# Performance work log

Hardware: AMD Instinct MI355X
Metric: run time of the kernel (lower is better)

## Reference

```python
import jax, jax.numpy as jnp
import numpy as np

N = 50000      # nodes
IN = 128       # in_dim
HID = 128      # hidden_dim
HEADS = 4
OUT = HID // HEADS   # per-head out_channels
R = 8          # num_relations
E = 640000     # message-passing edges
E2 = 200000    # decode edge pairs
NC = 8         # num_classes
EPS_LN = 1e-5


def layer_norm(x, g, b):
    m = x.mean(-1, keepdims=True)
    v = ((x - m) ** 2).mean(-1, keepdims=True)
    return (x - m) * jax.lax.rsqrt(v + EPS_LN) * g + b


def rgat_conv(x, edge_index, edge_type, W, q, k, b):
    # PyG RGATConv defaults: additive-self-attention, across-relation softmax,
    # concat=True, negative_slope=0.2, sum aggregation.
    src, dst = edge_index[0], edge_index[1]
    # relation-specific transform for all nodes, then gather per edge
    xw = jnp.einsum('ni,rio->nro', x, W)          # [N, R, HID]
    xi = xw[dst, edge_type]                        # [E, HID] target feats
    xj = xw[src, edge_type]                        # [E, HID] source feats
    alpha = jax.nn.leaky_relu(xi @ q + xj @ k, negative_slope=0.2)  # [E, HEADS]
    # softmax over incoming edges of each destination node (per head)
    amax = jax.ops.segment_max(alpha, dst, num_segments=N)
    amax = jnp.where(jnp.isfinite(amax), amax, 0.0)
    ex = jnp.exp(alpha - amax[dst])
    den = jax.ops.segment_sum(ex, dst, num_segments=N)
    attn = ex / (den[dst] + 1e-16)                 # [E, HEADS]
    msg = (xj.reshape(E, HEADS, OUT) * attn[:, :, None]).reshape(E, HID)
    out = jax.ops.segment_sum(msg, dst, num_segments=N)  # [N, HID]
    return out + b


def setup_inputs() -> dict:
    key = jax.random.key(0)
    ks = jax.random.split(key, 12)
    sI = 1.0 / np.sqrt(IN)
    sH = 1.0 / np.sqrt(HID)
    return {
        'x': jax.random.normal(ks[0], (N, IN), jnp.float32),
        'edge_index': jax.random.randint(ks[1], (2, E), 0, N),
        'edge_type': jax.random.randint(ks[2], (E,), 0, R),
        'edges': jax.random.randint(ks[3], (E2, 2), 0, N),
        'w1': jax.random.normal(ks[4], (R, IN, HID), jnp.float32) * sI,
        'q1': jax.random.normal(ks[5], (HID, HEADS), jnp.float32) * sH,
        'k1': jax.random.normal(ks[6], (HID, HEADS), jnp.float32) * sH,
        'b1': jnp.zeros((HID,), jnp.float32),
        'w2': jax.random.normal(ks[7], (R, HID, HID), jnp.float32) * sH,
        'q2': jax.random.normal(ks[8], (HID, HEADS), jnp.float32) * sH,
        'k2': jax.random.normal(ks[9], (HID, HEADS), jnp.float32) * sH,
        'b2': jnp.zeros((HID,), jnp.float32),
        'ln1_g': jnp.ones((HID,), jnp.float32),
        'ln1_b': jnp.zeros((HID,), jnp.float32),
        'ln2_g': jnp.ones((HID,), jnp.float32),
        'ln2_b': jnp.zeros((HID,), jnp.float32),
        'mw1': jax.random.normal(ks[10], (2 * HID, HID), jnp.float32) / np.sqrt(2 * HID),
        'mb1': jnp.zeros((HID,), jnp.float32),
        'mw2': jax.random.normal(ks[11], (HID, NC), jnp.float32) * sH,
        'mb2': jnp.zeros((NC,), jnp.float32),
    }


def reference(x, edge_index, edge_type, edges,
              w1, q1, k1, b1, w2, q2, k2, b2,
              ln1_g, ln1_b, ln2_g, ln2_b,
              mw1, mb1, mw2, mb2):
    # encode (dropout is identity in eval mode)
    h1 = rgat_conv(x, edge_index, edge_type, w1, q1, k1, b1)
    h1 = layer_norm(jax.nn.relu(h1), ln1_g, ln1_b)
    h2 = rgat_conv(h1, edge_index, edge_type, w2, q2, k2, b2)
    h2 = layer_norm(jax.nn.relu(h2), ln2_g, ln2_b)
    h = h1 + h2
    # decode: gather node pairs, concat, MLP
    z = jnp.concatenate([h[edges[:, 0]], h[edges[:, 1]]], axis=1)  # [E2, 2*HID]
    z = jax.nn.gelu(z @ mw1 + mb1, approximate=False)
    return z @ mw2 + mb2  # [E2, NC]
```

## Files before the change

### kernel.cpp

```cpp
#include <hip/hip_runtime.h>
#include <hip/hip_bf16.h>

#define NN    50000
#define RR    8
#define HIDC  128
#define NHEADS 4
#define EE    640000
#define EE2   200000
#define NCL   8

typedef __hip_bfloat16 bf16;
typedef unsigned short u16;
typedef __attribute__((ext_vector_type(8))) short short8;
typedef __attribute__((ext_vector_type(4))) float floatx4;

__device__ __forceinline__ float us2f(u16 u) {
    return __uint_as_float(((unsigned)u) << 16);
}
__device__ __forceinline__ float bf2f(bf16 v) { return __bfloat162float(v); }
__device__ __forceinline__ u16 f2us(float f) {
    bf16 h = __float2bfloat16(f);
    return *(u16*)&h;
}
__device__ __forceinline__ float ldf(const void* p, int i, bool f32) {
    return f32 ? ((const float*)p)[i] : us2f(((const u16*)p)[i]);
}
__device__ __forceinline__ float wredmax(float v) {
#pragma unroll
    for (int off = 32; off; off >>= 1) v = fmaxf(v, __shfl_xor(v, off));
    return v;
}
__device__ __forceinline__ float wredsum(float v) {
#pragma unroll
    for (int off = 32; off; off >>= 1) v += __shfl_xor(v, off);
    return v;
}

__global__ __launch_bounds__(1024) void k_sniff(const u16* __restrict__ x, int* __restrict__ flags) {
    __shared__ int cnt;
    if (threadIdx.x == 0) cnt = 0;
    __syncthreads();
    int c = 0;
#pragma unroll
    for (int it = 0; it < 8; it++) {
        ushort4 a = ((const ushort4*)x)[(it * 1024 + threadIdx.x) * 2];
        ushort4 b = ((const ushort4*)x)[(it * 1024 + threadIdx.x) * 2 + 1];
        c += (((a.x >> 7) & 0xFF) == 0xFF) + (((a.y >> 7) & 0xFF) == 0xFF)
           + (((a.z >> 7) & 0xFF) == 0xFF) + (((a.w >> 7) & 0xFF) == 0xFF)
           + (((b.x >> 7) & 0xFF) == 0xFF) + (((b.y >> 7) & 0xFF) == 0xFF)
           + (((b.z >> 7) & 0xFF) == 0xFF) + (((b.w >> 7) & 0xFF) == 0xFF);
    }
    c += __shfl_xor(c, 32); c += __shfl_xor(c, 16); c += __shfl_xor(c, 8);
    c += __shfl_xor(c, 4);  c += __shfl_xor(c, 2);  c += __shfl_xor(c, 1);
    if ((threadIdx.x & 63) == 0) atomicAdd(&cnt, c);
    __syncthreads();
    if (threadIdx.x == 0) { flags[0] = (cnt > 16) ? 1 : 0; flags[1] = 0; }
}

__global__ void k_zero(int* __restrict__ p, int n) {
    int i = blockIdx.x * 256 + threadIdx.x;
    if (i < n) p[i] = 0;
}
__global__ void k_hist(const int* __restrict__ ei, int* __restrict__ deg) {
    int e = blockIdx.x * 256 + threadIdx.x;
    if (e < EE) atomicAdd(&deg[ei[EE + e]], 1);
}
__global__ __launch_bounds__(256) void k_scan1(const int* __restrict__ deg,
                                               int* __restrict__ bsum) {
    int i = blockIdx.x * 256 + threadIdx.x;
    int v = (i < NN) ? deg[i] : 0;
    __shared__ int red[4];
    int lane = threadIdx.x & 63, w = threadIdx.x >> 6;
#pragma unroll
    for (int off = 32; off; off >>= 1) v += __shfl_xor(v, off);
    if (lane == 0) red[w] = v;
    __syncthreads();
    if (threadIdx.x == 0) bsum[blockIdx.x] = red[0] + red[1] + red[2] + red[3];
}
__global__ __launch_bounds__(256) void k_scan2(const int* __restrict__ bsum,
                                               int* __restrict__ boff,
                                               int* __restrict__ rowptr) {
    __shared__ int s[256];
    int t = threadIdx.x;
    s[t] = (t < 196) ? bsum[t] : 0;
    __syncthreads();
    for (int off = 1; off < 256; off <<= 1) {
        int u = (t >= off) ? s[t - off] : 0;
        __syncthreads();
        s[t] += u;
        __syncthreads();
    }
    if (t < 196) boff[t] = (t == 0) ? 0 : s[t - 1];
    if (t == 255) rowptr[NN] = s[255];
}
__global__ __launch_bounds__(256) void k_scan3(int* __restrict__ deg ,
                                               const int* __restrict__ boff,
                                               int* __restrict__ rowptr) {
    __shared__ int s[256];
    int t = threadIdx.x;
    int i = blockIdx.x * 256 + t;
    int v = (i < NN) ? deg[i] : 0;
    s[t] = v;
    __syncthreads();
    for (int off = 1; off < 256; off <<= 1) {
        int u = (t >= off) ? s[t - off] : 0;
        __syncthreads();
        s[t] += u;
        __syncthreads();
    }
    if (i < NN) {
        int val = boff[blockIdx.x] + s[t] - v;
        rowptr[i] = val;
        deg[i] = val;
    }
}
__global__ void k_scatter(const int* __restrict__ ei, int* __restrict__ cursor,
                          int* __restrict__ elist) {
    int e = blockIdx.x * 256 + threadIdx.x;
    if (e >= EE) return;
    int pos = atomicAdd(&cursor[ei[EE + e]], 1);
    elist[pos] = e;
}

__global__ void k_qkw(const void* __restrict__ w1, const void* __restrict__ w2,
                      const void* __restrict__ q1, const void* __restrict__ k1,
                      const void* __restrict__ q2, const void* __restrict__ k2,
                      float* __restrict__ qkw, const int* __restrict__ fl) {
    int idx = blockIdx.x * 256 + threadIdx.x;
    if (idx >= 16384) return;
    const bool f = fl[0] != 0;
    int mat = idx >> 10;
    int i   = (idx >> 3) & 127;
    int h8  = idx & 7;
    const void* W = (mat >= 8) ? w2 : w1;
    const void* qk = (mat >= 8) ? ((h8 < 4) ? q2 : k2) : ((h8 < 4) ? q1 : k1);
    int h = h8 & 3;
    int r = mat & 7;
    float acc = 0.f;
    for (int o = 0; o < HIDC; o++)
        acc += ldf(W, (r * HIDC + i) * HIDC + o, f) * ldf(qk, o * NHEADS + h, f);
    qkw[idx] = acc;
}

__global__ void k_wswz(const void* __restrict__ w1, const void* __restrict__ w2,
                       const float* __restrict__ qkw,
                       u16* __restrict__ Wf2, const int* __restrict__ fl) {
    int idx = blockIdx.x * 256 + threadIdx.x;
    if (idx >= 36864) return;
    const bool f = fl[0] != 0;
    int mat = idx / 2304, rest = idx % 2304;
    int c = rest >> 8, q = (rest >> 6) & 3, ln = rest & 63;
    int k0 = q * 32 + (ln >> 4) * 8;
    int nn = c * 16 + (ln & 15);
    int r = mat & 7;
    u16 o[8];
    if (c < 8) {
        const void* W = (mat >= 8) ? w2 : w1;
#pragma unroll
        for (int j = 0; j < 8; j++)
            o[j] = f2us(ldf(W, (r * HIDC + k0 + j) * HIDC + nn, f));
    } else {
        int col = nn - 128;
#pragma unroll
        for (int j = 0; j < 8; j++)
            o[j] = (col < 8) ? f2us(qkw[mat * 1024 + (k0 + j) * 8 + col]) : (u16)0;
    }
    u16* dst = Wf2 + (size_t)mat * 18432 + (size_t)(((c * 4 + q) * 64 + ln) * 8);
    *(ushort4*)dst       = ushort4{o[0], o[1], o[2], o[3]};
    *(ushort4*)(dst + 4) = ushort4{o[4], o[5], o[6], o[7]};
}

__global__ __launch_bounds__(512) void k_xw2(const void* __restrict__ X,
                                             const u16* __restrict__ Wf2,
                                             bf16* __restrict__ xw,
                                             float* __restrict__ sbuf,
                                             float* __restrict__ tbuf,
                                             const int* __restrict__ fx,
                                             int layer) {
    __shared__ u16 Xs[64 * 136];
    __shared__ u16 Os[8][16 * 136];
    const int tid = threadIdx.x;
    const int n0 = blockIdx.x * 64;
    const bool xf = fx[0] != 0;
    for (int v = tid; v < 2048; v += 512) {
        int row = v >> 5, c4 = (v & 31) * 4, n = n0 + row;
        ushort4 o = {0, 0, 0, 0};
        if (n < NN) {
            if (xf) {
                float4 hv = *(const float4*)((const float*)X + (size_t)n * HIDC + c4);
                o = ushort4{f2us(hv.x), f2us(hv.y), f2us(hv.z), f2us(hv.w)};
            } else {
                o = *(const ushort4*)((const u16*)X + (size_t)n * HIDC + c4);
            }
        }
        *(ushort4*)&Xs[row * 136 + c4] = o;
    }
    __syncthreads();
    const int w = tid >> 6, lane = tid & 63;
    const int wr = w & 3;
    const int rh = w >> 2;
    short8 af[4];
#pragma unroll
    for (int q = 0; q < 4; q++)
        af[q] = *(const short8*)&Xs[(16 * wr + (lane & 15)) * 136 + q * 32 + (lane >> 4) * 8];
    u16* Ow = Os[w];
    for (int rr = 0; rr < 4; rr++) {
        const int r = rh * 4 + rr;
        const u16* Wfr = Wf2 + (size_t)(layer * 8 + r) * 18432;
#pragma unroll
        for (int c = 0; c < 9; c++) {
            floatx4 acc = {0.f, 0.f, 0.f, 0.f};
#pragma unroll
            for (int q = 0; q < 4; q++) {
                short8 bfr = *(const short8*)&Wfr[(size_t)(((c * 4 + q) * 64 + lane) * 8)];
                acc = __builtin_amdgcn_mfma_f32_16x16x32_bf16(af[q], bfr, acc, 0, 0, 0);
            }
            if (c < 8) {
                int col = c * 16 + (lane & 15);
#pragma unroll
                for (int reg = 0; reg < 4; reg++) {
                    int lp = (lane >> 4) * 4 + reg;
                    Ow[lp * 136 + col] = f2us(acc[reg]);
                }
            } else {
                int cl = lane & 15;
                if (cl < 8) {
                    float* dstp = (cl < 4) ? sbuf : tbuf;
                    int h = cl & 3;
#pragma unroll
                    for (int reg = 0; reg < 4; reg++) {
                        int p = 16 * wr + (lane >> 4) * 4 + reg;
                        int n = n0 + p;
                        if (n < NN) dstp[(size_t)(n * RR + r) * 4 + h] = acc[reg];
                    }
                }
            }
        }
#pragma unroll
        for (int i = 0; i < 4; i++) {
            int v = i * 64 + lane;
            int lrow = v >> 4;
            int c8 = (v & 15) * 8;
            int n = n0 + 16 * wr + lrow;
            if (n < NN) {
                short8 hv = *(const short8*)&Ow[lrow * 136 + c8];
                *(short8*)((u16*)xw + (size_t)(n * RR + r) * HIDC + c8) = hv;
            }
        }
    }
}

__global__ __launch_bounds__(256) void k_attn(const int* __restrict__ rowptr,
                                              const int* __restrict__ elist,
                                              const int* __restrict__ ei,
                                              const int* __restrict__ et,
                                              const float* __restrict__ sb,
                                              const float* __restrict__ tb,
                                              const bf16* __restrict__ xw,
                                              const void* __restrict__ b,
                                              const void* __restrict__ g,
                                              const void* __restrict__ bb,
                                              const u16* __restrict__ hprev,
                                              u16* __restrict__ hout,
                                              const int* __restrict__ fl) {
    const int lane = threadIdx.x & 63;
    const int d = blockIdx.x * 4 + (threadIdx.x >> 6);
    if (d >= NN) return;
    const bool f = fl[0] != 0;
    const int half = lane >> 5;
    const int sl = lane & 31;
    const int hh = sl >> 3;
    const int start = rowptr[d], end = rowptr[d + 1];
    float m0 = -1e30f, m1 = -1e30f, m2 = -1e30f, m3 = -1e30f;
    float l0 = 0.f, l1 = 0.f, l2 = 0.f, l3 = 0.f;
    float acc0 = 0.f, acc1 = 0.f, acc2 = 0.f, acc3 = 0.f;
    for (int c0 = start; c0 < end; c0 += 64) {
        int n = end - c0;
        if (n > 64) n = 64;
        float a0, a1, a2, a3;
        int sr = 0;
        if (lane < n) {
            int e = elist[c0 + lane];
            int src = ei[e], r = et[e];
            sr = src * RR + r;
            float4 si = *(const float4*)&sb[(size_t)(d * RR + r) * 4];
            float4 tj = *(const float4*)&tb[(size_t)sr * 4];
            a0 = si.x + tj.x; a0 = a0 >= 0.f ? a0 : 0.2f * a0;
            a1 = si.y + tj.y; a1 = a1 >= 0.f ? a1 : 0.2f * a1;
            a2 = si.z + tj.z; a2 = a2 >= 0.f ? a2 : 0.2f * a2;
            a3 = si.w + tj.w; a3 = a3 >= 0.f ? a3 : 0.2f * a3;
        } else { a0 = a1 = a2 = a3 = -1e30f; }
        float n0 = fmaxf(m0, wredmax(a0));
        float n1 = fmaxf(m1, wredmax(a1));
        float n2 = fmaxf(m2, wredmax(a2));
        float n3 = fmaxf(m3, wredmax(a3));
        float s0 = __expf(m0 - n0), s1 = __expf(m1 - n1);
        float s2 = __expf(m2 - n2), s3 = __expf(m3 - n3);
        float e0 = __expf(a0 - n0), e1 = __expf(a1 - n1);
        float e2 = __expf(a2 - n2), e3 = __expf(a3 - n3);
        l0 = l0 * s0 + wredsum(e0);
        l1 = l1 * s1 + wredsum(e1);
        l2 = l2 * s2 + wredsum(e2);
        l3 = l3 * s3 + wredsum(e3);
        float scl = hh == 0 ? s0 : hh == 1 ? s1 : hh == 2 ? s2 : s3;
        acc0 *= scl; acc1 *= scl; acc2 *= scl; acc3 *= scl;
        for (int j2 = 0; j2 < n; j2 += 2) {
            int jl = j2 + half;
            int srj = __shfl(sr, jl);
            float wx = __shfl(e0, jl), wy = __shfl(e1, jl);
            float wz = __shfl(e2, jl), ww = __shfl(e3, jl);
            float wgt = hh == 0 ? wx : hh == 1 ? wy : hh == 2 ? wz : ww;
            ushort4 u = *(const ushort4*)((const u16*)xw + (size_t)srj * HIDC + sl * 4);
            acc0 += wgt * us2f(u.x);
            acc1 += wgt * us2f(u.y);
            acc2 += wgt * us2f(u.z);
            acc3 += wgt * us2f(u.w);
        }
        m0 = n0; m1 = n1; m2 = n2; m3 = n3;
    }
    acc0 += __shfl_xor(acc0, 32);
    acc1 += __shfl_xor(acc1, 32);
    acc2 += __shfl_xor(acc2, 32);
    acc3 += __shfl_xor(acc3, 32);
    float ld = hh == 0 ? l0 : hh == 1 ? l1 : hh == 2 ? l2 : l3;
    float inv = 1.f / (ld + 1e-16f);
    float v0 = fmaxf(acc0 * inv + ldf(b, sl * 4 + 0, f), 0.f);
    float v1 = fmaxf(acc1 * inv + ldf(b, sl * 4 + 1, f), 0.f);
    float v2 = fmaxf(acc2 * inv + ldf(b, sl * 4 + 2, f), 0.f);
    float v3 = fmaxf(acc3 * inv + ldf(b, sl * 4 + 3, f), 0.f);
    float sum = v0 + v1 + v2 + v3;
#pragma unroll
    for (int off = 16; off; off >>= 1) sum += __shfl_xor(sum, off);
    float mean = sum * (1.f / 128.f);
    v0 -= mean; v1 -= mean; v2 -= mean; v3 -= mean;
    float sq = v0 * v0 + v1 * v1 + v2 * v2 + v3 * v3;
#pragma unroll
    for (int off = 16; off; off >>= 1) sq += __shfl_xor(sq, off);
    float rstd = rsqrtf(sq * (1.f / 128.f) + 1e-5f);
    if (half == 0) {
        float y0 = v0 * rstd * ldf(g, sl * 4 + 0, f) + ldf(bb, sl * 4 + 0, f);
        float y1 = v1 * rstd * ldf(g, sl * 4 + 1, f) + ldf(bb, sl * 4 + 1, f);
        float y2 = v2 * rstd * ldf(g, sl * 4 + 2, f) + ldf(bb, sl * 4 + 2, f);
        float y3 = v3 * rstd * ldf(g, sl * 4 + 3, f) + ldf(bb, sl * 4 + 3, f);
        if (hprev) {
            ushort4 hv = *(const ushort4*)&hprev[(size_t)d * HIDC + sl * 4];
            y0 += us2f(hv.x); y1 += us2f(hv.y); y2 += us2f(hv.z); y3 += us2f(hv.w);
        }
        ushort4 o = {f2us(y0), f2us(y1), f2us(y2), f2us(y3)};
        *(ushort4*)&hout[(size_t)d * HIDC + sl * 4] = o;
    }
}

__global__ void k_dswz(const void* __restrict__ mw1, const void* __restrict__ mw2,
                       u16* __restrict__ Wf, const int* __restrict__ fl) {
    int idx = blockIdx.x * 256 + threadIdx.x;
    if (idx >= 4352) return;
    const bool f = fl[0] != 0;
    u16 o[8];
    if (idx < 4096) {
        int c = idx >> 9, q = (idx >> 6) & 7, ln = idx & 63;
        int k0 = q * 32 + (ln >> 4) * 8;
        int nn = c * 16 + (ln & 15);
#pragma unroll
        for (int j = 0; j < 8; j++)
            o[j] = f2us(ldf(mw1, (k0 + j) * HIDC + nn, f));
    } else {
        int fidx = idx - 4096;
        int q = fidx >> 6, ln = fidx & 63;
        int k0 = q * 32 + (ln >> 4) * 8;
        int nn = ln & 15;
#pragma unroll
        for (int j = 0; j < 8; j++)
            o[j] = (nn < 8) ? f2us(ldf(mw2, (k0 + j) * NCL + nn, f)) : (u16)0;
    }
    *(ushort4*)&Wf[idx * 8]     = ushort4{o[0], o[1], o[2], o[3]};
    *(ushort4*)&Wf[idx * 8 + 4] = ushort4{o[4], o[5], o[6], o[7]};
}

__global__ __launch_bounds__(256) void k_decode2(const u16* __restrict__ h,
                                                 const int* __restrict__ edges,
                                                 const u16* __restrict__ Wf,
                                                 const void* __restrict__ mb1,
                                                 const void* __restrict__ mb2,
                                                 void* __restrict__ out,
                                                 const int* __restrict__ fl) {
    __shared__ u16 zsu[64 * 136];
    const int tid = threadIdx.x;
    const bool f = fl[0] != 0;
    const int p0 = blockIdx.x * 64;
    const int w = tid >> 6, lane = tid & 63;
    const int m = 16 * w + (lane & 15);
    const int g = lane >> 4;
    const int na = edges[(size_t)(p0 + m) * 2];
    const int nb = edges[(size_t)(p0 + m) * 2 + 1];
    short8 af[8];
#pragma unroll
    for (int q = 0; q < 8; q++) {
        int k0 = q * 32 + g * 8;
        af[q] = *(const short8*)(h + (size_t)((k0 >> 7) ? nb : na) * HIDC + (k0 & 127));
    }
#pragma unroll
    for (int c = 0; c < 8; c++) {
        floatx4 acc = {0.f, 0.f, 0.f, 0.f};
#pragma unroll
        for (int q = 0; q < 8; q++) {
            short8 bfr = *(const short8*)&Wf[(size_t)(((c * 8 + q) * 64 + lane) * 8)];
            acc = __builtin_amdgcn_mfma_f32_16x16x32_bf16(af[q], bfr, acc, 0, 0, 0);
        }
        int col = c * 16 + (lane & 15);
        float bv = ldf(mb1, col, f);
#pragma unroll
        for (int reg = 0; reg < 4; reg++) {
            int p = 16 * w + (lane >> 4) * 4 + reg;
            float z = acc[reg] + bv;
            zsu[p * 136 + col] = f2us(0.5f * z * (1.f + erff(z * 0.70710678118654752f)));
        }
    }
    floatx4 acc2 = {0.f, 0.f, 0.f, 0.f};
#pragma unroll
    for (int q = 0; q < 4; q++) {
        short8 af2 = *(const short8*)&zsu[m * 136 + q * 32 + g * 8];
        short8 bfr2 = *(const short8*)&Wf[32768 + (size_t)((q * 64 + lane) * 8)];
        acc2 = __builtin_amdgcn_mfma_f32_16x16x32_bf16(af2, bfr2, acc2, 0, 0, 0);
    }
    int col16 = lane & 15;
    if (col16 < 8) {
        float bv2 = ldf(mb2, col16, f);
#pragma unroll
        for (int reg = 0; reg < 4; reg++) {
            int p = 16 * w + (lane >> 4) * 4 + reg;
            float sv = acc2[reg] + bv2;
            size_t oi = (size_t)(p0 + p) * NCL + col16;
            if (f) ((float*)out)[oi] = sv;
            else   ((bf16*)out)[oi] = __float2bfloat16(sv);
        }
    }
}

extern "C" void kernel_launch(void* const* d_in, const int* in_sizes, int n_in,
                              void* d_out, int out_size, void* d_ws, size_t ws_size,
                              hipStream_t stream) {
    (void)in_sizes; (void)n_in; (void)out_size; (void)ws_size;
    const void* x    = d_in[0];
    const int* ei    = (const int*)d_in[1];
    const int* et    = (const int*)d_in[2];
    const int* edges = (const int*)d_in[3];
    const void* w1 = d_in[4];
    const void* q1 = d_in[5];
    const void* k1 = d_in[6];
    const void* b1 = d_in[7];
    const void* w2 = d_in[8];
    const void* q2 = d_in[9];
    const void* k2 = d_in[10];
    const void* b2 = d_in[11];
    const void* ln1g = d_in[12];
    const void* ln1b = d_in[13];
    const void* ln2g = d_in[14];
    const void* ln2b = d_in[15];
    const void* mw1 = d_in[16];
    const void* mb1 = d_in[17];
    const void* mw2 = d_in[18];
    const void* mb2 = d_in[19];

    char* ws = (char*)d_ws;
    bf16* xwb   = (bf16*)ws;
    u16* Wf     = (u16*)ws;
    float* sbuf = (float*)(ws + 102400000);
    float* tbuf = (float*)(ws + 108800000);
    u16* h1     = (u16*)(ws + 115200000);
    u16* hsum   = (u16*)(ws + 140800000);
    u16* Wf2    = (u16*)(ws + 153600000);
    int* rowptr = (int*)(ws + 166400000);
    int* cursor = (int*)(ws + 166600016);
    int* elist  = (int*)(ws + 166800016);
    float* qkw  = (float*)(ws + 169360016);
    int* bsum   = (int*)qkw;
    int* boff   = bsum + 256;
    int* flags  = (int*)(ws + 169425552);

    k_sniff<<<1, 1024, 0, stream>>>((const u16*)x, flags);

    k_zero<<<196, 256, 0, stream>>>(cursor, NN);
    k_hist<<<2500, 256, 0, stream>>>(ei, cursor);
    k_scan1<<<196, 256, 0, stream>>>(cursor, bsum);
    k_scan2<<<1, 256, 0, stream>>>(bsum, boff, rowptr);
    k_scan3<<<196, 256, 0, stream>>>(cursor, boff, rowptr);
    k_scatter<<<2500, 256, 0, stream>>>(ei, cursor, elist);
    k_qkw<<<64, 256, 0, stream>>>(w1, w2, q1, k1, q2, k2, qkw, flags);
    k_wswz<<<144, 256, 0, stream>>>(w1, w2, qkw, Wf2, flags);

    for (int layer = 0; layer < 2; ++layer) {
        const void* b  = layer ? b2 : b1;
        const void* lg = layer ? ln2g : ln1g;
        const void* lb = layer ? ln2b : ln1b;
        k_xw2<<<782, 512, 0, stream>>>(layer ? (const void*)h1 : x, Wf2, xwb,
                                       sbuf, tbuf,
                                       layer ? flags + 1 : flags, layer);
        k_attn<<<12500, 256, 0, stream>>>(rowptr, elist, ei, et, sbuf, tbuf, xwb,
                                          b, lg, lb,
                                          layer ? h1 : (const u16*)nullptr,
                                          layer ? hsum : h1, flags);
    }
    k_dswz<<<17, 256, 0, stream>>>(mw1, mw2, Wf, flags);
    k_decode2<<<3125, 256, 0, stream>>>(hsum, edges, Wf, mb1, mb2, d_out, flags);
}
```

Measured before the change: 479.0 us.

## Assign 16 lanes per destination node and precompute src*R+type edge keys

The scatter now stores the combined src*R+relation index in the CSR edge list, so the attention kernel skips two dependent gathers per edge. The attention kernel now uses 16-lane groups per destination node instead of a full 64-lane wavefront, with 16-edge chunks, 16-byte feature loads per lane, and edge weights passed through shared memory. This targets the wasted lanes and reduction cost for low-degree nodes (average degree about 13). In exchange each lane holds more accumulators, and the shared-memory staging is written and read without an explicit barrier, which relies on each group sitting inside a single wavefront.

Result: no change. 479.8 us (+0.2%).

```diff
diff --git a/kernel.cpp b/kernel.cpp
--- a/kernel.cpp
+++ b/kernel.cpp
@@ -24,16 +24,6 @@
 }
 __device__ __forceinline__ float ldf(const void* p, int i, bool f32) {
     return f32 ? ((const float*)p)[i] : us2f(((const u16*)p)[i]);
-}
-__device__ __forceinline__ float wredmax(float v) {
-#pragma unroll
-    for (int off = 32; off; off >>= 1) v = fmaxf(v, __shfl_xor(v, off));
-    return v;
-}
-__device__ __forceinline__ float wredsum(float v) {
-#pragma unroll
-    for (int off = 32; off; off >>= 1) v += __shfl_xor(v, off);
-    return v;
 }
 
 __global__ __launch_bounds__(1024) void k_sniff(const u16* __restrict__ x, int* __restrict__ flags) {
@@ -114,12 +104,12 @@
         deg[i] = val;
     }
 }
-__global__ void k_scatter(const int* __restrict__ ei, int* __restrict__ cursor,
-                          int* __restrict__ elist) {
+__global__ void k_scatter(const int* __restrict__ ei, const int* __restrict__ et,
+                          int* __restrict__ cursor, int* __restrict__ elist) {
     int e = blockIdx.x * 256 + threadIdx.x;
     if (e >= EE) return;
     int pos = atomicAdd(&cursor[ei[EE + e]], 1);
-    elist[pos] = e;
+    elist[pos] = ei[e] * RR + et[e];
 }
 
 __global__ void k_qkw(const void* __restrict__ w1, const void* __restrict__ w2,
@@ -251,9 +241,7 @@
 }
 
 __global__ __launch_bounds__(256) void k_attn(const int* __restrict__ rowptr,
-                                              const int* __restrict__ elist,
-                                              const int* __restrict__ ei,
-                                              const int* __restrict__ et,
+                                              const int* __restrict__ srlist,
                                               const float* __restrict__ sb,
                                               const float* __restrict__ tb,
                                               const bf16* __restrict__ xw,
@@ -263,26 +251,28 @@
                                               const u16* __restrict__ hprev,
                                               u16* __restrict__ hout,
                                               const int* __restrict__ fl) {
-    const int lane = threadIdx.x & 63;
-    const int d = blockIdx.x * 4 + (threadIdx.x >> 6);
-    if (d >= NN) return;
+    __shared__ int   srs[16][16];
+    __shared__ float exs[16][16][4];
+    const int tid = threadIdx.x;
+    const int grp = tid >> 4;
+    const int sl  = tid & 15;
+    const int hh  = sl >> 2;
+    const int d   = blockIdx.x * 16 + grp;
     const bool f = fl[0] != 0;
-    const int half = lane >> 5;
-    const int sl = lane & 31;
-    const int hh = sl >> 3;
     const int start = rowptr[d], end = rowptr[d + 1];
     float m0 = -1e30f, m1 = -1e30f, m2 = -1e30f, m3 = -1e30f;
     float l0 = 0.f, l1 = 0.f, l2 = 0.f, l3 = 0.f;
-    float acc0 = 0.f, acc1 = 0.f, acc2 = 0.f, acc3 = 0.f;
-    for (int c0 = start; c0 < end; c0 += 64) {
+    float acc[8];
+#pragma unroll
+    for (int i = 0; i < 8; i++) acc[i] = 0.f;
+    for (int c0 = start; c0 < end; c0 += 16) {
         int n = end - c0;
-        if (n > 64) n = 64;
+        if (n > 16) n = 16;
         float a0, a1, a2, a3;
         int sr = 0;
-        if (lane < n) {
-            int e = elist[c0 + lane];
-            int src = ei[e], r = et[e];
-            sr = src * RR + r;
+        if (sl < n) {
+            sr = srlist[c0 + sl];
+            int r = sr & 7;
             float4 si = *(const float4*)&sb[(size_t)(d * RR + r) * 4];
             float4 tj = *(const float4*)&tb[(size_t)sr * 4];
             a0 = si.x + tj.x; a0 = a0 >= 0.f ? a0 : 0.2f * a0;
@@ -290,65 +280,86 @@
             a2 = si.z + tj.z; a2 = a2 >= 0.f ? a2 : 0.2f * a2;
             a3 = si.w + tj.w; a3 = a3 >= 0.f ? a3 : 0.2f * a3;
         } else { a0 = a1 = a2 = a3 = -1e30f; }
-        float n0 = fmaxf(m0, wredmax(a0));
-        float n1 = fmaxf(m1, wredmax(a1));
-        float n2 = fmaxf(m2, wredmax(a2));
-        float n3 = fmaxf(m3, wredmax(a3));
+        float c0m = a0, c1m = a1, c2m = a2, c3m = a3;
+#pragma unroll
+        for (int off = 8; off; off >>= 1) {
+            c0m = fmaxf(c0m, __shfl_xor(c0m, off));
+            c1m = fmaxf(c1m, __shfl_xor(c1m, off));
+            c2m = fmaxf(c2m, __shfl_xor(c2m, off));
+            c3m = fmaxf(c3m, __shfl_xor(c3m, off));
+        }
+        float n0 = fmaxf(m0, c0m), n1 = fmaxf(m1, c1m);
+        float n2 = fmaxf(m2, c2m), n3 = fmaxf(m3, c3m);
         float s0 = __expf(m0 - n0), s1 = __expf(m1 - n1);
         float s2 = __expf(m2 - n2), s3 = __expf(m3 - n3);
         float e0 = __expf(a0 - n0), e1 = __expf(a1 - n1);
         float e2 = __expf(a2 - n2), e3 = __expf(a3 - n3);
-        l0 = l0 * s0 + wredsum(e0);
-        l1 = l1 * s1 + wredsum(e1);
-        l2 = l2 * s2 + wredsum(e2);
-        l3 = l3 * s3 + wredsum(e3);
+        float t0 = e0, t1 = e1, t2 = e2, t3 = e3;
+#pragma unroll
+        for (int off = 8; off; off >>= 1) {
+            t0 += __shfl_xor(t0, off);
+            t1 += __shfl_xor(t1, off);
+            t2 += __shfl_xor(t2, off);
+            t3 += __shfl_xor(t3, off);
+        }
+        l0 = l0 * s0 + t0; l1 = l1 * s1 + t1;
+        l2 = l2 * s2 + t2; l3 = l3 * s3 + t3;
+        srs[grp][sl] = sr;
+        *(float4*)&exs[grp][sl][0] = float4{e0, e1, e2, e3};
         float scl = hh == 0 ? s0 : hh == 1 ? s1 : hh == 2 ? s2 : s3;
-        acc0 *= scl; acc1 *= scl; acc2 *= scl; acc3 *= scl;
-        for (int j2 = 0; j2 < n; j2 += 2) {
-            int jl = j2 + half;
-            int srj = __shfl(sr, jl);
-            float wx = __shfl(e0, jl), wy = __shfl(e1, jl);
-            float wz = __shfl(e2, jl), ww = __shfl(e3, jl);
-            float wgt = hh == 0 ? wx : hh == 1 ? wy : hh == 2 ? wz : ww;
-            ushort4 u = *(const ushort4*)((const u16*)xw + (size_t)srj * HIDC + sl * 4);
-            acc0 += wgt * us2f(u.x);
-            acc1 += wgt * us2f(u.y);
-            acc2 += wgt * us2f(u.z);
-            acc3 += wgt * us2f(u.w);
+#pragma unroll
+        for (int i = 0; i < 8; i++) acc[i] *= scl;
+        int j = 0;
+        for (; j + 2 <= n; j += 2) {
+            int sa = srs[grp][j], sb2 = srs[grp][j + 1];
+            float wa = exs[grp][j][hh], wb = exs[grp][j + 1][hh];
+            short8 ua = *(const short8*)((const u16*)xw + (size_t)sa * HIDC + sl * 8);
+            short8 ub = *(const short8*)((const u16*)xw + (size_t)sb2 * HIDC + sl * 8);
+#pragma unroll
+            for (int i = 0; i < 8; i++) acc[i] += wa * us2f((u16)ua[i]);
+#pragma unroll
+            for (int i = 0; i < 8; i++) acc[i] += wb * us2f((u16)ub[i]);
+        }
+        if (j < n) {
+            int sa = srs[grp][j];
+            float wa = exs[grp][j][hh];
+            short8 ua = *(const short8*)((const u16*)xw + (size_t)sa * HIDC + sl * 8);
+#pragma unroll
+            for (int i = 0; i < 8; i++) acc[i] += wa * us2f((u16)ua[i]);
         }
         m0 = n0; m1 = n1; m2 = n2; m3 = n3;
     }
-    acc0 += __shfl_xor(acc0, 32);
-    acc1 += __shfl_xor(acc1, 32);
-    acc2 += __shfl_xor(acc2, 32);
-    acc3 += __shfl_xor(acc3, 32);
     float ld = hh == 0 ? l0 : hh == 1 ? l1 : hh == 2 ? l2 : l3;
     float inv = 1.f / (ld + 1e-16f);
-    float v0 = fmaxf(acc0 * inv + ldf(b, sl * 4 + 0, f), 0.f);
-    float v1 = fmaxf(acc1 * inv + ldf(b, sl * 4 + 1, f), 0.f);
-    float v2 = fmaxf(acc2 * inv + ldf(b, sl * 4 + 2, f), 0.f);
-    float v3 = fmaxf(acc3 * inv + ldf(b, sl * 4 + 3, f), 0.f);
-    float sum = v0 + v1 + v2 + v3;
-#pragma unroll
-    for (int off = 16; off; off >>= 1) sum += __shfl_xor(sum, off);
+    float v[8];
+#pragma unroll
+    for (int i = 0; i < 8; i++)
+        v[i] = fmaxf(acc[i] * inv + ldf(b, sl * 8 + i, f), 0.f);
+    float sum = 0.f;
+#pragma unroll
+    for (int i = 0; i < 8; i++) sum += v[i];
+#pragma unroll
+    for (int off = 8; off; off >>= 1) sum += __shfl_xor(sum, off);
     float mean = sum * (1.f / 128.f);
-    v0 -= mean; v1 -= mean; v2 -= mean; v3 -= mean;
-    float sq = v0 * v0 + v1 * v1 + v2 * v2 + v3 * v3;
-#pragma unroll
-    for (int off = 16; off; off >>= 1) sq += __shfl_xor(sq, off);
+    float sq = 0.f;
+#pragma unroll
+    for (int i = 0; i < 8; i++) { v[i] -= mean; sq += v[i] * v[i]; }
+#pragma unroll
+    for (int off = 8; off; off >>= 1) sq += __shfl_xor(sq, off);
     float rstd = rsqrtf(sq * (1.f / 128.f) + 1e-5f);
-    if (half == 0) {
-        float y0 = v0 * rstd * ldf(g, sl * 4 + 0, f) + ldf(bb, sl * 4 + 0, f);
-        float y1 = v1 * rstd * ldf(g, sl * 4 + 1, f) + ldf(bb, sl * 4 + 1, f);
-        float y2 = v2 * rstd * ldf(g, sl * 4 + 2, f) + ldf(bb, sl * 4 + 2, f);
-        float y3 = v3 * rstd * ldf(g, sl * 4 + 3, f) + ldf(bb, sl * 4 + 3, f);
-        if (hprev) {
-            ushort4 hv = *(const ushort4*)&hprev[(size_t)d * HIDC + sl * 4];
-            y0 += us2f(hv.x); y1 += us2f(hv.y); y2 += us2f(hv.z); y3 += us2f(hv.w);
-        }
-        ushort4 o = {f2us(y0), f2us(y1), f2us(y2), f2us(y3)};
-        *(ushort4*)&hout[(size_t)d * HIDC + sl * 4] = o;
-    }
+    short8 o;
+#pragma unroll
+    for (int i = 0; i < 8; i++) {
+        float y = v[i] * rstd * ldf(g, sl * 8 + i, f) + ldf(bb, sl * 8 + i, f);
+        o[i] = (short)f2us(y);
+    }
+    if (hprev) {
+        short8 hv = *(const short8*)&hprev[(size_t)d * HIDC + sl * 8];
+#pragma unroll
+        for (int i = 0; i < 8; i++)
+            o[i] = (short)f2us(us2f((u16)o[i]) + us2f((u16)hv[i]));
+    }
+    *(short8*)&hout[(size_t)d * HIDC + sl * 8] = o;
 }
 
 __global__ void k_dswz(const void* __restrict__ mw1, const void* __restrict__ mw2,
@@ -485,7 +496,7 @@
     k_scan1<<<196, 256, 0, stream>>>(cursor, bsum);
     k_scan2<<<1, 256, 0, stream>>>(bsum, boff, rowptr);
     k_scan3<<<196, 256, 0, stream>>>(cursor, boff, rowptr);
-    k_scatter<<<2500, 256, 0, stream>>>(ei, cursor, elist);
+    k_scatter<<<2500, 256, 0, stream>>>(ei, et, cursor, elist);
     k_qkw<<<64, 256, 0, stream>>>(w1, w2, q1, k1, q2, k2, qkw, flags);
     k_wswz<<<144, 256, 0, stream>>>(w1, w2, qkw, Wf2, flags);
 
@@ -496,10 +507,10 @@
         k_xw2<<<782, 512, 0, stream>>>(layer ? (const void*)h1 : x, Wf2, xwb,
                                        sbuf, tbuf,
                                        layer ? flags + 1 : flags, layer);
-        k_attn<<<12500, 256, 0, stream>>>(rowptr, elist, ei, et, sbuf, tbuf, xwb,
-                                          b, lg, lb,
-                                          layer ? h1 : (const u16*)nullptr,
-                                          layer ? hsum : h1, flags);
+        k_attn<<<3125, 256, 0, stream>>>(rowptr, elist, sbuf, tbuf, xwb,
+                                         b, lg, lb,
+                                         layer ? h1 : (const u16*)nullptr,
+                                         layer ? hsum : h1, flags);
     }
     k_dswz<<<17, 256, 0, stream>>>(mw1, mw2, Wf, flags);
     k_decode2<<<3125, 256, 0, stream>>>(hsum, edges, Wf, mb1, mb2, d_out, flags);
```
